# Kernel tuning notes

Measured on AMD Instinct MI355X. Metric: run time of the kernel, lower is better.

Reference implementation:

```python
import jax, jax.numpy as jnp
import numpy as np

SPATIAL_SHAPES = np.array([[100, 100], [50, 50], [25, 25], [13, 13]], dtype=np.int64)
LEVEL_START = np.concatenate([[0], np.cumsum(SPATIAL_SHAPES[:, 0] * SPATIAL_SHAPES[:, 1])[:-1]])
L_TOK = int((SPATIAL_SHAPES[:, 0] * SPATIAL_SHAPES[:, 1]).sum())  # 13294
B, D_MODEL, N_HEADS, N_LEVELS, N_POINTS, D_FFN = 4, 256, 8, 4, 4, 1024
HEAD_DIM = D_MODEL // N_HEADS


def setup_inputs() -> dict:
    key = jax.random.key(0)
    ks = jax.random.split(key, 16)
    p = lambda k, s: jax.random.normal(k, s, jnp.float32) * 0.02
    return {
        'src': jax.random.normal(ks[0], (B, L_TOK, D_MODEL), jnp.float32),
        'src2': jax.random.normal(ks[1], (B, L_TOK, D_MODEL), jnp.float32),
        'pos': jax.random.normal(ks[2], (B, L_TOK, D_MODEL), jnp.float32),
        'memory_pos': jax.random.normal(ks[3], (B, L_TOK, D_MODEL), jnp.float32),
        'value_w': p(ks[4], (D_MODEL, D_MODEL)), 'value_b': jnp.zeros((D_MODEL,), jnp.float32),
        'off_w': p(ks[5], (D_MODEL, N_HEADS * N_LEVELS * N_POINTS * 2)),
        'off_b': p(ks[6], (N_HEADS * N_LEVELS * N_POINTS * 2,)),
        'aw_w': p(ks[7], (D_MODEL, N_HEADS * N_LEVELS * N_POINTS)),
        'aw_b': jnp.zeros((N_HEADS * N_LEVELS * N_POINTS,), jnp.float32),
        'out_w': p(ks[8], (D_MODEL, D_MODEL)), 'out_b': jnp.zeros((D_MODEL,), jnp.float32),
        'ln_g': jnp.ones((D_MODEL,), jnp.float32), 'ln_b': jnp.zeros((D_MODEL,), jnp.float32),
        'lin1_w': p(ks[9], (D_MODEL, D_FFN)), 'lin1_b': jnp.zeros((D_FFN,), jnp.float32),
        'lin2_w': p(ks[10], (D_FFN, D_MODEL)), 'lin2_b': jnp.zeros((D_MODEL,), jnp.float32),
    }


def _layer_norm(x, g, b, eps=1e-5):
    mu = jnp.mean(x, -1, keepdims=True)
    var = jnp.mean(jnp.square(x - mu), -1, keepdims=True)
    return (x - mu) * jax.lax.rsqrt(var + eps) * g + b


def _reference_points():
    # per get_reference_points: normalized (x, y) centers per src level -> [1, L_TOK, 1, 2]
    pts = []
    for H_, W_ in SPATIAL_SHAPES:
        ry, rx = np.meshgrid(np.linspace(0.5, H_ - 0.5, H_) / H_,
                             np.linspace(0.5, W_ - 0.5, W_) / W_, indexing='ij')
        pts.append(np.stack([rx.reshape(-1), ry.reshape(-1)], -1))
    return jnp.asarray(np.concatenate(pts, 0), jnp.float32)[None, :, None, :]


def _bilinear(value, loc, H_, W_):
    # value: [N, H*W, D]; loc: [N, S, 2] normalized in [0,1]
    # matches F.grid_sample(align_corners=False, padding_mode='zeros') with grid = 2*loc-1
    x = loc[..., 0] * W_ - 0.5
    y = loc[..., 1] * H_ - 0.5
    x0 = jnp.floor(x)
    y0 = jnp.floor(y)
    wx1 = x - x0
    wy1 = y - y0
    out = jnp.zeros(value.shape[:1] + loc.shape[1:2] + value.shape[2:], value.dtype)
    for dy, wy in ((0, 1.0 - wy1), (1, wy1)):
        for dx, wx in ((0, 1.0 - wx1), (1, wx1)):
            xi = x0 + dx
            yi = y0 + dy
            valid = (xi >= 0) & (xi < W_) & (yi >= 0) & (yi < H_)
            idx = (jnp.clip(yi, 0, H_ - 1) * W_ + jnp.clip(xi, 0, W_ - 1)).astype(jnp.int32)
            v = jnp.take_along_axis(value, idx[..., None], axis=1)
            out = out + v * (wx * wy * valid)[..., None]
    return out


def _ms_deform_attn(query, ref, memory, value_w, value_b, off_w, off_b, aw_w, aw_b, out_w, out_b):
    Bq, Lq = query.shape[0], query.shape[1]
    value = (memory @ value_w + value_b).reshape(Bq, -1, N_HEADS, HEAD_DIM)
    offs = (query @ off_w + off_b).reshape(Bq, Lq, N_HEADS, N_LEVELS, N_POINTS, 2)
    norm = jnp.asarray(SPATIAL_SHAPES[:, ::-1].copy(), jnp.float32)  # (W, H) per level
    loc = ref[:, :, None, :, None, :] + offs / norm[None, None, None, :, None, :]
    aw = jax.nn.softmax((query @ aw_w + aw_b).reshape(Bq, Lq, N_HEADS, N_LEVELS * N_POINTS), -1)
    aw = aw.reshape(Bq, Lq, N_HEADS, N_LEVELS, N_POINTS)
    acc = jnp.zeros((Bq, Lq, N_HEADS, HEAD_DIM), query.dtype)
    for l in range(N_LEVELS):
        H_, W_ = int(SPATIAL_SHAPES[l, 0]), int(SPATIAL_SHAPES[l, 1])
        s = int(LEVEL_START[l])
        v = value[:, s:s + H_ * W_].transpose(0, 2, 1, 3).reshape(Bq * N_HEADS, H_ * W_, HEAD_DIM)
        ll = loc[:, :, :, l].transpose(0, 2, 1, 3, 4).reshape(Bq * N_HEADS, Lq * N_POINTS, 2)
        samp = _bilinear(v, ll, H_, W_).reshape(Bq, N_HEADS, Lq, N_POINTS, HEAD_DIM)
        acc = acc + jnp.einsum('bhqpd,bqhp->bqhd', samp, aw[:, :, :, l])
    return acc.reshape(Bq, Lq, D_MODEL) @ out_w + out_b


def reference(src, src2, pos, memory_pos, value_w, value_b, off_w, off_b, aw_w, aw_b,
              out_w, out_b, ln_g, ln_b, lin1_w, lin1_b, lin2_w, lin2_b):
    ref = _reference_points()
    q = src + pos
    mem = src2 + memory_pos
    attn = _ms_deform_attn(q, ref, mem, value_w, value_b, off_w, off_b, aw_w, aw_b, out_w, out_b)
    # residual + norm2 (dropout is identity in eval)
    x = _layer_norm(src + attn, ln_g, ln_b)
    # FFN; note the original re-uses norm2 (it was assigned twice in __init__)
    ffn = jax.nn.relu(x @ lin1_w + lin1_b) @ lin2_w + lin2_b
    return _layer_norm(x + ffn, ln_g, ln_b)
```

## Files before the change

kernel.cpp:

```cpp
#include <hip/hip_runtime.h>
#include <math.h>

#define L_TOKN 13294
#define BATCHN 4
#define NTOK (BATCHN * L_TOKN)
#define NTOKP 53248
#define DMODEL 256
#define DFFN 1024

typedef __attribute__((ext_vector_type(8))) short short8;
typedef __attribute__((ext_vector_type(4))) float f32x4;
typedef __attribute__((ext_vector_type(2))) float f32x2;

__device__ __forceinline__ ushort f2b(float f) {
    uint u = __float_as_uint(f);
    u += 0x7fff + ((u >> 16) & 1);
    return (ushort)(u >> 16);
}
__device__ __forceinline__ float b2f(uint h) {
    return __uint_as_float(h << 16);
}

__global__ __launch_bounds__(256) void prep_k(
    const float* __restrict__ s1, const float* __restrict__ p1,
    const float* __restrict__ s2, const float* __restrict__ p2,
    ushort* __restrict__ o1, ushort* __restrict__ o2,
    const float* __restrict__ w0, const float* __restrict__ w1,
    const float* __restrict__ w2, const float* __restrict__ w3,
    const float* __restrict__ w4, const float* __restrict__ w5,
    ushort* __restrict__ wtb, int n4)
{
    int i = blockIdx.x * 256 + threadIdx.x;
    if (i < 2 * n4) {
        const float* a; const float* b; ushort* o; int j;
        if (i < n4) { a = s1; b = p1; o = o1; j = i; }
        else        { a = s2; b = p2; o = o2; j = i - n4; }
        float4 va = ((const float4*)a)[j];
        float4 vb = ((const float4*)b)[j];
        ushort4 r;
        r.x = f2b(va.x + vb.x); r.y = f2b(va.y + vb.y);
        r.z = f2b(va.z + vb.z); r.w = f2b(va.w + vb.w);
        ((ushort4*)o)[j] = r;
        return;
    }
    int i2 = i - 2 * n4;
    const float* w; int Nd; size_t off; int j;
    if      (i2 < 65536)  { w = w0; Nd = 256;  off = 0;      j = i2; }
    else if (i2 < 131072) { w = w1; Nd = 256;  off = 65536;  j = i2 - 65536; }
    else if (i2 < 163840) { w = w2; Nd = 128;  off = 131072; j = i2 - 131072; }
    else if (i2 < 229376) { w = w3; Nd = 256;  off = 163840; j = i2 - 163840; }
    else if (i2 < 491520) { w = w4; Nd = 1024; off = 229376; j = i2 - 229376; }
    else if (i2 < 753664) { w = w5; Nd = 256;  off = 491520; j = i2 - 491520; }
    else return;
    int Kd = (i2 < 491520) ? 256 : 1024;
    int k = j / Nd, n = j - k * Nd;
    wtb[off + (size_t)n * Kd + k] = f2b(w[j]);
}

__device__ __forceinline__ void gemm_core(
    const ushort* __restrict__ A, const ushort* __restrict__ Wt,
    const float* __restrict__ bias, const float* __restrict__ bias2,
    float* __restrict__ Cf, ushort* __restrict__ Cb,
    int M, int N, int K, int relu, int nsplit, int m0, int n0)
{
    __shared__ ushort lds[16384];

    const int t  = threadIdx.x;
    const int wv = t >> 6, ln_ = t & 63;
    const int wr = wv >> 1, wc = wv & 1;
    const int fr = ln_ & 15;
    const int kg = ln_ >> 4;

    f32x4 acc[4][4];
    #pragma unroll
    for (int i = 0; i < 4; i++)
        #pragma unroll
        for (int j = 0; j < 4; j++) acc[i][j] = (f32x4)0.0f;

    int aoff[4], boff[4];
    #pragma unroll
    for (int i = 0; i < 4; i++) {
        aoff[i] = (wr * 64 + i * 16 + fr) * 32 + kg * 8;
        boff[i] = 4096 + (wc * 64 + i * 16 + fr) * 32 + kg * 8;
    }

#define STAGE(pbuf, k0) do {                                                       \
    _Pragma("unroll")                                                              \
    for (int ii = 0; ii < 2; ii++) {                                               \
        int c = (wv * 2 + ii) * 64 + ln_;                                          \
        int m = c >> 2, s = c & 3;                                                 \
        const ushort* sa = A  + (size_t)(m0 + m) * K + (k0) + s * 8;               \
        const ushort* sb = Wt + (size_t)(n0 + m) * K + (k0) + s * 8;               \
        __builtin_amdgcn_global_load_lds(                                          \
            (const __attribute__((address_space(1))) unsigned int*)sa,             \
            (__attribute__((address_space(3))) unsigned int*)&lds[(pbuf) * 8192 + (wv * 2 + ii) * 512], \
            16, 0, 0);                                                             \
        __builtin_amdgcn_global_load_lds(                                          \
            (const __attribute__((address_space(1))) unsigned int*)sb,             \
            (__attribute__((address_space(3))) unsigned int*)&lds[(pbuf) * 8192 + 4096 + (wv * 2 + ii) * 512], \
            16, 0, 0);                                                             \
    }                                                                              \
} while (0)

    const int nk = K >> 5;
    STAGE(0, 0);
    __syncthreads();

    for (int ks = 0; ks < nk; ks++) {
        const int p = ks & 1;
        if (ks + 1 < nk) STAGE(p ^ 1, (ks + 1) << 5);

        short8 af[4], bf[4];
        const int pb = p * 8192;
        #pragma unroll
        for (int i = 0; i < 4; i++) {
            af[i] = *(const short8*)&lds[pb + aoff[i]];
            bf[i] = *(const short8*)&lds[pb + boff[i]];
        }
        #pragma unroll
        for (int i = 0; i < 4; i++)
            #pragma unroll
            for (int j = 0; j < 4; j++)
                acc[i][j] = __builtin_amdgcn_mfma_f32_16x16x32_bf16(af[i], bf[j], acc[i][j], 0, 0, 0);

        if (ks + 1 < nk) __syncthreads();
    }
#undef STAGE

    #pragma unroll
    for (int i = 0; i < 4; i++) {
        #pragma unroll
        for (int j = 0; j < 4; j++) {
            int col = n0 + wc * 64 + j * 16 + fr;
            float bv = (col < nsplit) ? bias[col] : bias2[col - nsplit];
            #pragma unroll
            for (int e = 0; e < 4; e++) {
                int row = m0 + wr * 64 + i * 16 + kg * 4 + e;
                if (row >= M) continue;
                float v = acc[i][j][e] + bv;
                if (relu) v = fmaxf(v, 0.f);
                if (Cf) Cf[(size_t)row * N + col] = v;
                if (Cb) Cb[(size_t)row * N + col] = f2b(v);
            }
        }
    }
}

__global__ __launch_bounds__(256) void mgemm_k(
    const ushort* __restrict__ A, const ushort* __restrict__ Wt,
    const float* __restrict__ bias, const float* __restrict__ bias2,
    float* __restrict__ Cf, ushort* __restrict__ Cb,
    int M, int N, int K, int relu, int nsplit)
{
    gemm_core(A, Wt, bias, bias2, Cf, Cb, M, N, K, relu, nsplit,
              blockIdx.y * 128, blockIdx.x * 128);
}

__global__ __launch_bounds__(256) void projs_k(
    const ushort* __restrict__ memb, const ushort* __restrict__ qb,
    const ushort* __restrict__ value_wt, const ushort* __restrict__ offaw_wt,
    const float* __restrict__ value_b, const float* __restrict__ off_b,
    const float* __restrict__ aw_b,
    ushort* __restrict__ vb, ushort* __restrict__ offawb)
{
    const int x = blockIdx.x;
    const int m0 = blockIdx.y * 128;
    const ushort* A; const ushort* Wt; const float* b1; const float* b2;
    ushort* Cb; int N, n0;
    if (x < 2) { A = memb; Wt = value_wt; b1 = value_b; b2 = value_b;
                 Cb = vb; N = 256; n0 = x * 128; }
    else       { A = qb;   Wt = offaw_wt; b1 = off_b;   b2 = aw_b;
                 Cb = offawb; N = 384; n0 = (x - 2) * 128; }
    gemm_core(A, Wt, b1, b2, nullptr, Cb, NTOK, N, 256, 0, 256, m0, n0);
}

__global__ __launch_bounds__(256) void deform_k(
    const ushort* __restrict__ Vb,
    const ushort* __restrict__ OFFAW,
    ushort* __restrict__ OUTb)
{
    __shared__ uint4 pw_idx[4][2][136];
    __shared__ uint2 pw_w[4][2][136];

    const int t = threadIdx.x;
    const int wv = t >> 6, lane = t & 63;
    const int tok0 = blockIdx.x * 8 + wv * 2;

    const int HWc[4] = {100, 50, 25, 13};
    const int STc[4] = {0, 10000, 12500, 13125};

    const int ppb = lane & 15;
    const int lvb = ppb >> 2;
    #pragma unroll
    for (int it = 0; it < 4; it++) {
        int tk = it >> 1;
        int h  = ((it & 1) << 2) + (lane >> 4);
        int row = tok0 + tk;
        int b = row / L_TOKN;
        int l = row - b * L_TOKN;
        int st_q, Wq;
        if      (l < 10000) { st_q = 0;     Wq = 100; }
        else if (l < 12500) { st_q = 10000; Wq = 50;  }
        else if (l < 13125) { st_q = 12500; Wq = 25;  }
        else                { st_q = 13125; Wq = 13;  }
        int li = l - st_q;
        int rowi = li / Wq;
        int coli = li - rowi * Wq;
        float rx = (coli + 0.5f) / (float)Wq;
        float ry = (rowi + 0.5f) / (float)Wq;

        const size_t rbase = (size_t)row * 384;
        uint oxy = *(const uint*)(OFFAW + rbase + h * 32 + ppb * 2);
        float ox = b2f(oxy & 0xffffu);
        float oy = b2f(oxy >> 16);
        float lg = b2f((uint)OFFAW[rbase + 256 + h * 16 + ppb]);
        float mx = lg;
        #pragma unroll
        for (int o = 8; o; o >>= 1) mx = fmaxf(mx, __shfl_xor(mx, o));
        float ex = __expf(lg - mx);
        float sm = ex;
        #pragma unroll
        for (int o = 8; o; o >>= 1) sm += __shfl_xor(sm, o);
        float aw = ex / sm;

        int Wl = HWc[lvb], stl = STc[lvb];
        float Wlf = (float)Wl;
        float x = (rx + ox / Wlf) * Wlf - 0.5f;
        float y = (ry + oy / Wlf) * Wlf - 0.5f;
        float x0f = floorf(x), y0f = floorf(y);
        float wx1 = x - x0f, wy1 = y - y0f;
        float wx0 = 1.f - wx1, wy0 = 1.f - wy1;
        int x0 = (int)x0f, y0 = (int)y0f;
        bool vx0 = (x0 >= 0) & (x0 < Wl);
        bool vx1 = (x0 + 1 >= 0) & (x0 + 1 < Wl);
        bool vy0 = (y0 >= 0) & (y0 < Wl);
        bool vy1 = (y0 + 1 >= 0) & (y0 + 1 < Wl);
        int cx0 = min(max(x0, 0), Wl - 1), cx1 = min(max(x0 + 1, 0), Wl - 1);
        int cy0 = min(max(y0, 0), Wl - 1), cy1 = min(max(y0 + 1, 0), Wl - 1);
        uint gb = (uint)(b * L_TOKN + stl);
        uint4 o4;
        o4.x = (gb + cy0 * Wl + cx0) * 512u;
        o4.y = (gb + cy0 * Wl + cx1) * 512u;
        o4.z = (gb + cy1 * Wl + cx0) * 512u;
        o4.w = (gb + cy1 * Wl + cx1) * 512u;
        float w00 = wx0 * wy0 * aw * (float)(vx0 & vy0);
        float w10 = wx1 * wy0 * aw * (float)(vx1 & vy0);
        float w01 = wx0 * wy1 * aw * (float)(vx0 & vy1);
        float w11 = wx1 * wy1 * aw * (float)(vx1 & vy1);
        uint2 wp;
        wp.x = (uint)f2b(w00) | ((uint)f2b(w10) << 16);
        wp.y = (uint)f2b(w01) | ((uint)f2b(w11) << 16);
        pw_idx[wv][tk][h * 17 + ppb] = o4;
        pw_w[wv][tk][h * 17 + ppb]   = wp;
    }

    asm volatile("s_waitcnt lgkmcnt(0)" ::: "memory");
    __builtin_amdgcn_sched_barrier(0);

    const int tk = lane >> 5;
    const int h  = (lane >> 2) & 7;
    const int dq = lane & 3;
    const int row = tok0 + tk;
    const uint choff = (uint)(h * 64 + dq * 16);
    const char* __restrict__ vbase = (const char*)Vb;

    f32x2 acc2[4];
    #pragma unroll
    for (int k = 0; k < 4; k++) acc2[k] = (f32x2)0.0f;

    #pragma unroll 8
    for (int pq = 0; pq < 16; pq++) {
        uint4 o4 = pw_idx[wv][tk][h * 17 + pq];
        uint2 wp = pw_w[wv][tk][h * 17 + pq];
        float w00 = b2f(wp.x & 0xffffu);
        float w10 = __uint_as_float(wp.x & 0xffff0000u);
        float w01 = b2f(wp.y & 0xffffu);
        float w11 = __uint_as_float(wp.y & 0xffff0000u);
        uint4 v00 = *(const uint4*)(vbase + o4.x + choff);
        uint4 v10 = *(const uint4*)(vbase + o4.y + choff);
        uint4 v01 = *(const uint4*)(vbase + o4.z + choff);
        uint4 v11 = *(const uint4*)(vbase + o4.w + choff);
        const uint* p00 = (const uint*)&v00;
        const uint* p10 = (const uint*)&v10;
        const uint* p01 = (const uint*)&v01;
        const uint* p11 = (const uint*)&v11;
        #pragma unroll
        for (int k = 0; k < 4; k++) {
            f32x2 a0, a1, a2, a3;
            a0.x = __uint_as_float(p00[k] << 16); a0.y = __uint_as_float(p00[k] & 0xffff0000u);
            a1.x = __uint_as_float(p10[k] << 16); a1.y = __uint_as_float(p10[k] & 0xffff0000u);
            a2.x = __uint_as_float(p01[k] << 16); a2.y = __uint_as_float(p01[k] & 0xffff0000u);
            a3.x = __uint_as_float(p11[k] << 16); a3.y = __uint_as_float(p11[k] & 0xffff0000u);
            acc2[k] += a0 * w00 + a1 * w10 + a2 * w01 + a3 * w11;
        }
    }
    ushort4 olo, ohi;
    olo.x = f2b(acc2[0].x); olo.y = f2b(acc2[0].y);
    olo.z = f2b(acc2[1].x); olo.w = f2b(acc2[1].y);
    ohi.x = f2b(acc2[2].x); ohi.y = f2b(acc2[2].y);
    ohi.z = f2b(acc2[3].x); ohi.w = f2b(acc2[3].y);
    ushort* op = OUTb + (size_t)row * 256 + h * 32 + dq * 8;
    *(ushort4*)op = olo;
    *(ushort4*)(op + 4) = ohi;
}

__global__ __launch_bounds__(256) void ln_k(
    const float* __restrict__ af, const ushort* __restrict__ ab,
    const float* __restrict__ bf2, const ushort* __restrict__ bb2,
    const float* __restrict__ g, const float* __restrict__ bta,
    float* __restrict__ of, ushort* __restrict__ ob)
{
    const int r = blockIdx.x * 4 + (threadIdx.x >> 6);
    const int lane = threadIdx.x & 63;
    float4 v;
    if (af) {
        v = *((const float4*)(af + (size_t)r * 256) + lane);
    } else {
        ushort4 u = *((const ushort4*)(ab + (size_t)r * 256) + lane);
        v.x = b2f(u.x); v.y = b2f(u.y); v.z = b2f(u.z); v.w = b2f(u.w);
    }
    if (bf2) {
        float4 v2 = *((const float4*)(bf2 + (size_t)r * 256) + lane);
        v.x += v2.x; v.y += v2.y; v.z += v2.z; v.w += v2.w;
    } else if (bb2) {
        ushort4 u = *((const ushort4*)(bb2 + (size_t)r * 256) + lane);
        v.x += b2f(u.x); v.y += b2f(u.y); v.z += b2f(u.z); v.w += b2f(u.w);
    }
    float s = v.x + v.y + v.z + v.w;
    #pragma unroll
    for (int o = 32; o; o >>= 1) s += __shfl_xor(s, o);
    float mu = s * (1.f / 256.f);
    float4 d; d.x = v.x - mu; d.y = v.y - mu; d.z = v.z - mu; d.w = v.w - mu;
    float s2 = d.x * d.x + d.y * d.y + d.z * d.z + d.w * d.w;
    #pragma unroll
    for (int o = 32; o; o >>= 1) s2 += __shfl_xor(s2, o);
    float rstd = rsqrtf(s2 * (1.f / 256.f) + 1e-5f);
    float4 gg = ((const float4*)g)[lane];
    float4 bb = ((const float4*)bta)[lane];
    float4 out;
    out.x = d.x * rstd * gg.x + bb.x;
    out.y = d.y * rstd * gg.y + bb.y;
    out.z = d.z * rstd * gg.z + bb.z;
    out.w = d.w * rstd * gg.w + bb.w;
    if (of) *((float4*)(of + (size_t)r * 256) + lane) = out;
    if (ob) {
        ushort4 o4;
        o4.x = f2b(out.x); o4.y = f2b(out.y); o4.z = f2b(out.z); o4.w = f2b(out.w);
        *((ushort4*)(ob + (size_t)r * 256) + lane) = o4;
    }
}

extern "C" void kernel_launch(void* const* d_in, const int* in_sizes, int n_in,
                              void* d_out, int out_size, void* d_ws, size_t ws_size,
                              hipStream_t stream)
{
    const float* src     = (const float*)d_in[0];
    const float* src2    = (const float*)d_in[1];
    const float* pos     = (const float*)d_in[2];
    const float* mpos    = (const float*)d_in[3];
    const float* value_w = (const float*)d_in[4];
    const float* value_b = (const float*)d_in[5];
    const float* off_w   = (const float*)d_in[6];
    const float* off_b   = (const float*)d_in[7];
    const float* aw_w    = (const float*)d_in[8];
    const float* aw_b    = (const float*)d_in[9];
    const float* out_w   = (const float*)d_in[10];
    const float* out_b   = (const float*)d_in[11];
    const float* ln_g    = (const float*)d_in[12];
    const float* ln_b    = (const float*)d_in[13];
    const float* lin1_w  = (const float*)d_in[14];
    const float* lin1_b  = (const float*)d_in[15];
    const float* lin2_w  = (const float*)d_in[16];
    const float* lin2_b  = (const float*)d_in[17];

    float* outp = (float*)d_out;
    char*  w8   = (char*)d_ws;

    const size_t SLAB = (size_t)NTOKP * 256 * 2;
    const size_t OASZ = (size_t)NTOKP * 384 * 2;
    const size_t HSZ  = (size_t)NTOKP * 1024 * 2;
    ushort* wtb    = (ushort*)(w8);
    ushort* offawb = (ushort*)(w8 + 1572864);
    ushort* qb     = (ushort*)(w8 + 1572864 + OASZ);
    ushort* vb     = (ushort*)(w8 + 1572864 + OASZ + SLAB);
    ushort* memb   = (ushort*)(w8 + 1572864 + HSZ);
    ushort* attb   = (ushort*)(w8 + 1572864 + HSZ + SLAB);

    ushort* hidb   = offawb;
    ushort* bufXb  = memb;
    ushort* projb  = vb;
    ushort* ffn2b  = attb;

    ushort* value_wt = wtb;
    ushort* offaw_wt = wtb + 65536;
    ushort* out_wt   = wtb + 163840;
    ushort* lin1_wt  = wtb + 229376;
    ushort* lin2_wt  = wtb + 491520;

    const dim3 blk(256);
    const int n4 = NTOK * DMODEL / 4;
    const int prep_total = 2 * n4 + 753664;
    prep_k<<<(prep_total + 255) / 256, blk, 0, stream>>>(
        src, pos, src2, mpos, qb, memb,
        value_w, off_w, aw_w, out_w, lin1_w, lin2_w, wtb, n4);

    const int mt = NTOKP / 128;
    projs_k<<<dim3(5, mt), blk, 0, stream>>>(memb, qb, value_wt, offaw_wt,
                                             value_b, off_b, aw_b, vb, offawb);

    deform_k<<<dim3(NTOK / 8), blk, 0, stream>>>(vb, offawb, attb);

    mgemm_k<<<dim3(2, mt), blk, 0, stream>>>(attb, out_wt, out_b, nullptr,
                                             nullptr, projb, NTOK, 256, 256, 0, 256);
    ln_k<<<dim3(NTOK / 4), blk, 0, stream>>>(nullptr, projb, src, nullptr,
                                             ln_g, ln_b, nullptr, bufXb);

    mgemm_k<<<dim3(8, mt), blk, 0, stream>>>(bufXb, lin1_wt, lin1_b, nullptr,
                                             nullptr, hidb, NTOK, DFFN, DMODEL, 1, DFFN);
    mgemm_k<<<dim3(2, mt), blk, 0, stream>>>(hidb, lin2_wt, lin2_b, nullptr,
                                             nullptr, ffn2b, NTOK, DMODEL, DFFN, 0, DMODEL);

    ln_k<<<dim3(NTOK / 4), blk, 0, stream>>>(nullptr, ffn2b, nullptr, bufXb,
                                             ln_g, ln_b, outp, nullptr);
}
```

Before: 421.8 us.

## Replace LDS-staged GEMM with single-wave register-direct 64x64 tiles

The shared-memory double-buffered 128x128 GEMM with four waves is replaced by one wave per 64x64 tile. Each wave loads A and W fragments straight from global memory into registers, double-buffers them in registers, and runs a fully unrolled K loop specialised on K. This removes LDS traffic and block barriers. In exchange, operand reuse across waves through LDS is lost, so global and L2 traffic roughly doubles, and the fragment loads are strided.

```diff
diff --git a/kernel.cpp b/kernel.cpp
--- a/kernel.cpp
+++ b/kernel.cpp
@@ -57,19 +57,25 @@
     wtb[off + (size_t)n * Kd + k] = f2b(w[j]);
 }
 
-__device__ __forceinline__ void gemm_core(
+template <int NK>
+__device__ __forceinline__ void gemm_core_reg(
     const ushort* __restrict__ A, const ushort* __restrict__ Wt,
     const float* __restrict__ bias, const float* __restrict__ bias2,
     float* __restrict__ Cf, ushort* __restrict__ Cb,
-    int M, int N, int K, int relu, int nsplit, int m0, int n0)
-{
-    __shared__ ushort lds[16384];
-
-    const int t  = threadIdx.x;
-    const int wv = t >> 6, ln_ = t & 63;
-    const int wr = wv >> 1, wc = wv & 1;
-    const int fr = ln_ & 15;
-    const int kg = ln_ >> 4;
+    int M, int N, int relu, int nsplit, int m0, int n0)
+{
+    constexpr int K = NK * 32;
+    const int lane = threadIdx.x & 63;
+    const int fr = lane & 15;
+    const int kg = lane >> 4;
+
+    const ushort* ap[4];
+    const ushort* bp[4];
+    #pragma unroll
+    for (int i = 0; i < 4; i++) {
+        ap[i] = A  + (size_t)(m0 + i * 16 + fr) * K + kg * 8;
+        bp[i] = Wt + (size_t)(n0 + i * 16 + fr) * K + kg * 8;
+    }
 
     f32x4 acc[4][4];
     #pragma unroll
@@ -77,65 +83,55 @@
         #pragma unroll
         for (int j = 0; j < 4; j++) acc[i][j] = (f32x4)0.0f;
 
-    int aoff[4], boff[4];
+    short8 a0[4], b0[4], a1[4], b1[4];
     #pragma unroll
     for (int i = 0; i < 4; i++) {
-        aoff[i] = (wr * 64 + i * 16 + fr) * 32 + kg * 8;
-        boff[i] = 4096 + (wc * 64 + i * 16 + fr) * 32 + kg * 8;
-    }
-
-#define STAGE(pbuf, k0) do {                                                       \
-    _Pragma("unroll")                                                              \
-    for (int ii = 0; ii < 2; ii++) {                                               \
-        int c = (wv * 2 + ii) * 64 + ln_;                                          \
-        int m = c >> 2, s = c & 3;                                                 \
-        const ushort* sa = A  + (size_t)(m0 + m) * K + (k0) + s * 8;               \
-        const ushort* sb = Wt + (size_t)(n0 + m) * K + (k0) + s * 8;               \
-        __builtin_amdgcn_global_load_lds(                                          \
-            (const __attribute__((address_space(1))) unsigned int*)sa,             \
-            (__attribute__((address_space(3))) unsigned int*)&lds[(pbuf) * 8192 + (wv * 2 + ii) * 512], \
-            16, 0, 0);                                                             \
-        __builtin_amdgcn_global_load_lds(                                          \
-            (const __attribute__((address_space(1))) unsigned int*)sb,             \
-            (__attribute__((address_space(3))) unsigned int*)&lds[(pbuf) * 8192 + 4096 + (wv * 2 + ii) * 512], \
-            16, 0, 0);                                                             \
-    }                                                                              \
-} while (0)
-
-    const int nk = K >> 5;
-    STAGE(0, 0);
-    __syncthreads();
-
-    for (int ks = 0; ks < nk; ks++) {
-        const int p = ks & 1;
-        if (ks + 1 < nk) STAGE(p ^ 1, (ks + 1) << 5);
-
-        short8 af[4], bf[4];
-        const int pb = p * 8192;
-        #pragma unroll
-        for (int i = 0; i < 4; i++) {
-            af[i] = *(const short8*)&lds[pb + aoff[i]];
-            bf[i] = *(const short8*)&lds[pb + boff[i]];
+        a0[i] = *(const short8*)(ap[i]);
+        b0[i] = *(const short8*)(bp[i]);
+    }
+
+    #pragma unroll
+    for (int ks = 0; ks < NK; ks++) {
+        if ((ks & 1) == 0) {
+            if (ks + 1 < NK) {
+                const int off = (ks + 1) * 32;
+                #pragma unroll
+                for (int i = 0; i < 4; i++) {
+                    a1[i] = *(const short8*)(ap[i] + off);
+                    b1[i] = *(const short8*)(bp[i] + off);
+                }
+            }
+            #pragma unroll
+            for (int i = 0; i < 4; i++)
+                #pragma unroll
+                for (int j = 0; j < 4; j++)
+                    acc[i][j] = __builtin_amdgcn_mfma_f32_16x16x32_bf16(a0[i], b0[j], acc[i][j], 0, 0, 0);
+        } else {
+            if (ks + 1 < NK) {
+                const int off = (ks + 1) * 32;
+                #pragma unroll
+                for (int i = 0; i < 4; i++) {
+                    a0[i] = *(const short8*)(ap[i] + off);
+                    b0[i] = *(const short8*)(bp[i] + off);
+                }
+            }
+            #pragma unroll
+            for (int i = 0; i < 4; i++)
+                #pragma unroll
+                for (int j = 0; j < 4; j++)
+                    acc[i][j] = __builtin_amdgcn_mfma_f32_16x16x32_bf16(a1[i], b1[j], acc[i][j], 0, 0, 0);
         }
-        #pragma unroll
-        for (int i = 0; i < 4; i++)
-            #pragma unroll
-            for (int j = 0; j < 4; j++)
-                acc[i][j] = __builtin_amdgcn_mfma_f32_16x16x32_bf16(af[i], bf[j], acc[i][j], 0, 0, 0);
-
-        if (ks + 1 < nk) __syncthreads();
-    }
-#undef STAGE
+    }
 
     #pragma unroll
     for (int i = 0; i < 4; i++) {
         #pragma unroll
         for (int j = 0; j < 4; j++) {
-            int col = n0 + wc * 64 + j * 16 + fr;
+            int col = n0 + j * 16 + fr;
             float bv = (col < nsplit) ? bias[col] : bias2[col - nsplit];
             #pragma unroll
             for (int e = 0; e < 4; e++) {
-                int row = m0 + wr * 64 + i * 16 + kg * 4 + e;
+                int row = m0 + i * 16 + kg * 4 + e;
                 if (row >= M) continue;
                 float v = acc[i][j][e] + bv;
                 if (relu) v = fmaxf(v, 0.f);
@@ -146,17 +142,21 @@
     }
 }
 
-__global__ __launch_bounds__(256) void mgemm_k(
+__global__ __launch_bounds__(64) void mgemm_k(
     const ushort* __restrict__ A, const ushort* __restrict__ Wt,
     const float* __restrict__ bias, const float* __restrict__ bias2,
     float* __restrict__ Cf, ushort* __restrict__ Cb,
     int M, int N, int K, int relu, int nsplit)
 {
-    gemm_core(A, Wt, bias, bias2, Cf, Cb, M, N, K, relu, nsplit,
-              blockIdx.y * 128, blockIdx.x * 128);
-}
-
-__global__ __launch_bounds__(256) void projs_k(
+    const int m0 = blockIdx.y * 64;
+    const int n0 = blockIdx.x * 64;
+    if (K == 256)
+        gemm_core_reg<8>(A, Wt, bias, bias2, Cf, Cb, M, N, relu, nsplit, m0, n0);
+    else
+        gemm_core_reg<32>(A, Wt, bias, bias2, Cf, Cb, M, N, relu, nsplit, m0, n0);
+}
+
+__global__ __launch_bounds__(64) void projs_k(
     const ushort* __restrict__ memb, const ushort* __restrict__ qb,
     const ushort* __restrict__ value_wt, const ushort* __restrict__ offaw_wt,
     const float* __restrict__ value_b, const float* __restrict__ off_b,
@@ -164,14 +164,13 @@
     ushort* __restrict__ vb, ushort* __restrict__ offawb)
 {
     const int x = blockIdx.x;
-    const int m0 = blockIdx.y * 128;
-    const ushort* A; const ushort* Wt; const float* b1; const float* b2;
-    ushort* Cb; int N, n0;
-    if (x < 2) { A = memb; Wt = value_wt; b1 = value_b; b2 = value_b;
-                 Cb = vb; N = 256; n0 = x * 128; }
-    else       { A = qb;   Wt = offaw_wt; b1 = off_b;   b2 = aw_b;
-                 Cb = offawb; N = 384; n0 = (x - 2) * 128; }
-    gemm_core(A, Wt, b1, b2, nullptr, Cb, NTOK, N, 256, 0, 256, m0, n0);
+    const int m0 = blockIdx.y * 64;
+    if (x < 4)
+        gemm_core_reg<8>(memb, value_wt, value_b, value_b, nullptr, vb,
+                         NTOK, 256, 0, 256, m0, x * 64);
+    else
+        gemm_core_reg<8>(qb, offaw_wt, off_b, aw_b, nullptr, offawb,
+                         NTOK, 384, 0, 256, m0, (x - 4) * 64);
 }
 
 __global__ __launch_bounds__(256) void deform_k(
@@ -398,27 +397,28 @@
     ushort* lin2_wt  = wtb + 491520;
 
     const dim3 blk(256);
+    const dim3 wblk(64);
     const int n4 = NTOK * DMODEL / 4;
     const int prep_total = 2 * n4 + 753664;
     prep_k<<<(prep_total + 255) / 256, blk, 0, stream>>>(
         src, pos, src2, mpos, qb, memb,
         value_w, off_w, aw_w, out_w, lin1_w, lin2_w, wtb, n4);
 
-    const int mt = NTOKP / 128;
-    projs_k<<<dim3(5, mt), blk, 0, stream>>>(memb, qb, value_wt, offaw_wt,
-                                             value_b, off_b, aw_b, vb, offawb);
+    const int mt64 = NTOKP / 64;
+    projs_k<<<dim3(10, mt64), wblk, 0, stream>>>(memb, qb, value_wt, offaw_wt,
+                                                 value_b, off_b, aw_b, vb, offawb);
 
     deform_k<<<dim3(NTOK / 8), blk, 0, stream>>>(vb, offawb, attb);
 
-    mgemm_k<<<dim3(2, mt), blk, 0, stream>>>(attb, out_wt, out_b, nullptr,
-                                             nullptr, projb, NTOK, 256, 256, 0, 256);
+    mgemm_k<<<dim3(4, mt64), wblk, 0, stream>>>(attb, out_wt, out_b, nullptr,
+                                                nullptr, projb, NTOK, 256, 256, 0, 256);
     ln_k<<<dim3(NTOK / 4), blk, 0, stream>>>(nullptr, projb, src, nullptr,
                                              ln_g, ln_b, nullptr, bufXb);
 
-    mgemm_k<<<dim3(8, mt), blk, 0, stream>>>(bufXb, lin1_wt, lin1_b, nullptr,
-                                             nullptr, hidb, NTOK, DFFN, DMODEL, 1, DFFN);
-    mgemm_k<<<dim3(2, mt), blk, 0, stream>>>(hidb, lin2_wt, lin2_b, nullptr,
-                                             nullptr, ffn2b, NTOK, DMODEL, DFFN, 0, DMODEL);
+    mgemm_k<<<dim3(16, mt64), wblk, 0, stream>>>(bufXb, lin1_wt, lin1_b, nullptr,
+                                                 nullptr, hidb, NTOK, DFFN, DMODEL, 1, DFFN);
+    mgemm_k<<<dim3(4, mt64), wblk, 0, stream>>>(hidb, lin2_wt, lin2_b, nullptr,
+                                                nullptr, ffn2b, NTOK, DMODEL, DFFN, 0, DMODEL);
 
     ln_k<<<dim3(NTOK / 4), blk, 0, stream>>>(nullptr, ffn2b, nullptr, bufXb,
                                              ln_g, ln_b, outp, nullptr);
```

New measurement: 563.8 us. +33.7%, slower.
